# Performance work log

Hardware: AMD Instinct MI355X
Metric: run time of the kernel (lower is better)

## Reference

```python
import math
import jax, jax.numpy as jnp
import numpy as np

DIM = 1024
DIM_QK = 128
DIM_V = 1024
CHUNK = 512
NUM_BUCKETS = 32
MAX_DISTANCE = 128


def _rel_pos_bucket(n_q, n_k):
    # causal T5 bucketing on the chunk-local grid
    q_pos = jnp.arange(n_q, dtype=jnp.int32)
    k_pos = jnp.arange(n_k, dtype=jnp.int32)
    rel = k_pos[None, :] - q_pos[:, None]          # [i, j]
    n = jnp.maximum(-rel, 0)                        # distance into the past
    max_exact = NUM_BUCKETS // 2
    is_small = n < max_exact
    n_f = jnp.maximum(n, 1).astype(jnp.float32)     # safe log
    val_large = max_exact + jnp.log(n_f / max_exact) / math.log(MAX_DISTANCE / max_exact) * (NUM_BUCKETS - max_exact)
    val_large = jnp.minimum(val_large, NUM_BUCKETS - 1)
    bucket = jnp.where(is_small, n.astype(jnp.float32), val_large)
    return bucket.astype(jnp.int32)                 # [i, j]


def setup_inputs() -> dict:
    key = jax.random.key(0)
    ks = jax.random.split(key, 6)
    b, s = 8, 4096
    x = jax.random.normal(ks[0], (b, s, DIM), dtype=jnp.float32)
    # Dense(dim_qk) / Dense(dim_value) params (glorot-ish scale)
    Wqk = jax.random.normal(ks[1], (DIM, DIM_QK), dtype=jnp.float32) * (1.0 / math.sqrt(DIM))
    bqk = jnp.zeros((DIM_QK,), dtype=jnp.float32)
    Wv = jax.random.normal(ks[2], (DIM, DIM_V), dtype=jnp.float32) * (1.0 / math.sqrt(DIM))
    bv = jnp.zeros((DIM_V,), dtype=jnp.float32)
    # OffsetScale: gamma ~ N(0, 0.02), beta = 0, heads=2
    gamma = jax.random.normal(ks[3], (2, DIM_QK), dtype=jnp.float32) * 0.02
    beta = jnp.zeros((2, DIM_QK), dtype=jnp.float32)
    # T5 relative position bias embedding table [num_buckets, 1]
    rel_emb = jax.random.normal(ks[4], (NUM_BUCKETS, 1), dtype=jnp.float32) * 0.05
    return {"x": x, "Wqk": Wqk, "bqk": bqk, "Wv": Wv, "bv": bv,
            "gamma": gamma, "beta": beta, "rel_emb": rel_emb}


def reference(x, Wqk, bqk, Wv, bv, gamma, beta, rel_emb):
    b, s, dim = x.shape
    qk = jax.nn.swish(x @ Wqk + bqk)                # [b, s, dqk]
    v = jax.nn.swish(x @ Wv + bv)                   # [b, s, dv]
    # OffsetScale with 2 heads -> q, k
    os = qk[..., None, :] * gamma + beta            # [b, s, 2, dqk]
    q, k = os[..., 0, :], os[..., 1, :]
    # chunk: [b, nk, c, z] (block-diagonal attention within chunks)
    c = CHUNK
    nk = s // c
    q = q.reshape(b, nk, c, DIM_QK)
    k = k.reshape(b, nk, c, DIM_QK)
    vc = v.reshape(b, nk, c, DIM_V)
    scale = dim ** (-0.5)                           # NOTE: input dim, faithful to source
    sim = jnp.einsum('bkiz,bkjz->bkij', q, k) * scale
    # T5 rel-pos bias on the chunk-local (c, c) grid, scaled by dim_qk ** 0.5
    bucket = _rel_pos_bucket(c, c)
    bias = rel_emb[bucket, 0] * (DIM_QK ** 0.5)     # [c, c]
    sim = sim + bias
    # causal mask: strictly-upper (future) positions -> -inf
    future = jnp.triu(jnp.ones((c, c), dtype=bool), k=1)
    sim = jnp.where(future, -jnp.inf, sim)
    attn = jax.nn.softmax(sim, axis=-1)
    out = jnp.einsum('bkij,bkjz->bkiz', attn, vc)
    return out.reshape(b, s, DIM_V)
```

## Files before the change

kernel.cpp:

```cpp
#include <hip/hip_runtime.h>
#include <hip/hip_bf16.h>

using bf16x8 = __attribute__((ext_vector_type(8))) short;
using f32x4  = __attribute__((ext_vector_type(4))) float;
typedef unsigned short u16;

#define SEQ_TOT 32768
#define NCHUNK  64
#define SQRT128 11.313708498984761f

__device__ __forceinline__ u16 f2bf(float f) {
  unsigned u = __builtin_bit_cast(unsigned, f);
  u += 0x7fffu + ((u >> 16) & 1u);
  return (u16)(u >> 16);
}

__device__ __forceinline__ float swishf(float c) {
  return c / (1.0f + __expf(-c));
}

__global__ __launch_bounds__(256) void prep_wqkt(const float* __restrict__ Wqk,
                                                 u16* __restrict__ Wqkt) {
  int t = blockIdx.x * 256 + threadIdx.x;
  int n = t >> 10, k = t & 1023;
  Wqkt[t] = f2bf(Wqk[(size_t)k * 128 + n]);
}

__global__ __launch_bounds__(256) void prep_wvt(const float* __restrict__ Wv,
                                                u16* __restrict__ Wvt) {
  int t = blockIdx.x * 256 + threadIdx.x;
  int n = t >> 10, k = t & 1023;
  Wvt[t] = f2bf(Wv[(size_t)k * 1024 + n]);
}

__global__ __launch_bounds__(512) void prep_bias(const float* __restrict__ rel_emb,
                                                 float* __restrict__ bias_tab) {
  int d = threadIdx.x;
  int b;
  if (d < 16) {
    b = d;
  } else {
    float v = 16.0f + __logf((float)d * 0.0625f) * (16.0f / 2.0794415416798357f);
    b = (int)v;
    if (b > 31) b = 31;
  }
  bias_tab[d] = rel_emb[b] * SQRT128;
}

__global__ __launch_bounds__(256, 2) void proj_kernel(
    const float* __restrict__ x,
    const u16* __restrict__ Wqkt, const u16* __restrict__ Wvt,
    const float* __restrict__ bqk, const float* __restrict__ bv,
    const float* __restrict__ gamma, const float* __restrict__ beta,
    u16* __restrict__ qm, u16* __restrict__ km, u16* __restrict__ vt) {
  __shared__ u16 a_lds[128][40];
  __shared__ u16 b_lds[128][40];
  const int tid = threadIdx.x;
  const int lane = tid & 63;
  const int wid = tid >> 6;
  const int wm = wid >> 1, wn = wid & 1;
  const int m0 = blockIdx.x * 128;
  const int nb = blockIdx.y;
  const u16* Wt = (nb == 0) ? Wqkt : (Wvt + (size_t)(nb - 1) * 128 * 1024);

  f32x4 acc[4][4];
#pragma unroll
  for (int i = 0; i < 4; i++)
#pragma unroll
    for (int j = 0; j < 4; j++) acc[i][j] = f32x4{0.f, 0.f, 0.f, 0.f};

  const int srow = tid >> 1;
  const int shalf = (tid & 1) * 16;

  for (int kt = 0; kt < 32; ++kt) {
    const int k0 = kt * 32;
    __syncthreads();
    {
      const float* src = x + (size_t)(m0 + srow) * 1024 + k0 + shalf;
      float4 f0 = *(const float4*)(src);
      float4 f1 = *(const float4*)(src + 4);
      float4 f2 = *(const float4*)(src + 8);
      float4 f3 = *(const float4*)(src + 12);
      uint4 p0, p1;
      p0.x = f2bf(f0.x) | ((unsigned)f2bf(f0.y) << 16);
      p0.y = f2bf(f0.z) | ((unsigned)f2bf(f0.w) << 16);
      p0.z = f2bf(f1.x) | ((unsigned)f2bf(f1.y) << 16);
      p0.w = f2bf(f1.z) | ((unsigned)f2bf(f1.w) << 16);
      p1.x = f2bf(f2.x) | ((unsigned)f2bf(f2.y) << 16);
      p1.y = f2bf(f2.z) | ((unsigned)f2bf(f2.w) << 16);
      p1.z = f2bf(f3.x) | ((unsigned)f2bf(f3.y) << 16);
      p1.w = f2bf(f3.z) | ((unsigned)f2bf(f3.w) << 16);
      *(uint4*)&a_lds[srow][shalf] = p0;
      *(uint4*)&a_lds[srow][shalf + 8] = p1;
    }
    {
      const u16* src = Wt + (size_t)srow * 1024 + k0 + shalf;
      uint4 w0 = *(const uint4*)(src);
      uint4 w1 = *(const uint4*)(src + 8);
      *(uint4*)&b_lds[srow][shalf] = w0;
      *(uint4*)&b_lds[srow][shalf + 8] = w1;
    }
    __syncthreads();
    bf16x8 af[4], bfr[4];
#pragma unroll
    for (int mi = 0; mi < 4; mi++)
      af[mi] = *(const bf16x8*)&a_lds[wm * 64 + mi * 16 + (lane & 15)][8 * (lane >> 4)];
#pragma unroll
    for (int ni = 0; ni < 4; ni++)
      bfr[ni] = *(const bf16x8*)&b_lds[wn * 64 + ni * 16 + (lane & 15)][8 * (lane >> 4)];
#pragma unroll
    for (int mi = 0; mi < 4; mi++)
#pragma unroll
      for (int ni = 0; ni < 4; ni++)
        acc[mi][ni] = __builtin_amdgcn_mfma_f32_16x16x32_bf16(af[mi], bfr[ni], acc[mi][ni], 0, 0, 0);
  }

  if (nb == 0) {
#pragma unroll
    for (int ni = 0; ni < 4; ni++) {
      const int nn = wn * 64 + ni * 16 + (lane & 15);
      const float bb = bqk[nn];
      const float g0 = gamma[nn], g1 = gamma[128 + nn];
      const float be0 = beta[nn], be1 = beta[128 + nn];
#pragma unroll
      for (int mi = 0; mi < 4; mi++) {
#pragma unroll
        for (int r = 0; r < 4; r++) {
          const int m = m0 + wm * 64 + mi * 16 + (lane >> 4) * 4 + r;
          const float s = swishf(acc[mi][ni][r] + bb);
          qm[(size_t)m * 128 + nn] = f2bf(s * g0 + be0);
          km[(size_t)m * 128 + nn] = f2bf(s * g1 + be1);
        }
      }
    }
  } else {
#pragma unroll
    for (int ni = 0; ni < 4; ni++) {
      const int z = (nb - 1) * 128 + wn * 64 + ni * 16 + (lane & 15);
      const float bb = bv[z];
#pragma unroll
      for (int mi = 0; mi < 4; mi++) {
        const int m = m0 + wm * 64 + mi * 16 + (lane >> 4) * 4;
        const int chunkid = m >> 9;
        const int j = m & 511;
        ushort4 pk;
        pk.x = f2bf(swishf(acc[mi][ni][0] + bb));
        pk.y = f2bf(swishf(acc[mi][ni][1] + bb));
        pk.z = f2bf(swishf(acc[mi][ni][2] + bb));
        pk.w = f2bf(swishf(acc[mi][ni][3] + bb));
        *(ushort4*)&vt[((size_t)chunkid * 1024 + z) * 512 + j] = pk;
      }
    }
  }
}

__global__ __launch_bounds__(256, 2) void score_kernel(
    const u16* __restrict__ qm, const u16* __restrict__ km,
    const float* __restrict__ bias_tab, u16* __restrict__ P) {
  __shared__ u16 k_lds[64][136];
  const int tid = threadIdx.x;
  const int lane = tid & 63;
  const int wid = tid >> 6;
  const int qt = blockIdx.x;
  const int ch = blockIdx.y;

  bf16x8 qf[4];
  {
    const int r = ch * 512 + qt * 64 + wid * 16 + (lane & 15);
    const u16* qp = qm + (size_t)r * 128 + 8 * (lane >> 4);
#pragma unroll
    for (int kk = 0; kk < 4; kk++) qf[kk] = *(const bf16x8*)(qp + kk * 32);
  }

  f32x4 acc[32];
#pragma unroll
  for (int i = 0; i < 32; i++) acc[i] = f32x4{0.f, 0.f, 0.f, 0.f};

  const int srow = tid >> 2;
  const int soff = (tid & 3) * 32;

#pragma unroll
  for (int kt = 0; kt < 8; ++kt) {
    if (kt <= qt) {
      __syncthreads();
      {
        const u16* src = km + (size_t)(ch * 512 + kt * 64 + srow) * 128 + soff;
        uint4 w0 = *(const uint4*)(src);
        uint4 w1 = *(const uint4*)(src + 8);
        uint4 w2 = *(const uint4*)(src + 16);
        uint4 w3 = *(const uint4*)(src + 24);
        *(uint4*)&k_lds[srow][soff] = w0;
        *(uint4*)&k_lds[srow][soff + 8] = w1;
        *(uint4*)&k_lds[srow][soff + 16] = w2;
        *(uint4*)&k_lds[srow][soff + 24] = w3;
      }
      __syncthreads();
#pragma unroll
      for (int jt = 0; jt < 4; jt++) {
#pragma unroll
        for (int kk = 0; kk < 4; kk++) {
          bf16x8 bfr = *(const bf16x8*)&k_lds[jt * 16 + (lane & 15)][kk * 32 + 8 * (lane >> 4)];
          acc[kt * 4 + jt] =
              __builtin_amdgcn_mfma_f32_16x16x32_bf16(qf[kk], bfr, acc[kt * 4 + jt], 0, 0, 0);
        }
      }
    }
  }

  const float scale = 0.03125f;
  const int jbase = lane & 15;
  const int nct = (qt + 1) * 4;

#pragma unroll
  for (int r = 0; r < 4; r++) {
    const int i = qt * 64 + wid * 16 + (lane >> 4) * 4 + r;
    float mx = -INFINITY;
#pragma unroll
    for (int ct = 0; ct < 32; ++ct) {
      if (ct < nct) {
        const int j = ct * 16 + jbase;
        float val = (j <= i) ? (acc[ct][r] * scale + bias_tab[i - j]) : -INFINITY;
        acc[ct][r] = val;
        mx = fmaxf(mx, val);
      }
    }
#pragma unroll
    for (int d = 1; d < 16; d <<= 1) mx = fmaxf(mx, __shfl_xor(mx, d));
    float sum = 0.f;
#pragma unroll
    for (int ct = 0; ct < 32; ++ct) {
      if (ct < nct) {
        float e = __expf(acc[ct][r] - mx);
        acc[ct][r] = e;
        sum += e;
      }
    }
#pragma unroll
    for (int d = 1; d < 16; d <<= 1) sum += __shfl_xor(sum, d);
    const float inv = 1.0f / sum;
    const size_t base = ((size_t)ch * 512 + i) * 512;
#pragma unroll
    for (int ct = 0; ct < 32; ++ct) {
      u16 pv = (ct < nct) ? f2bf(acc[ct][r] * inv) : (u16)0;
      P[base + ct * 16 + jbase] = pv;
    }
  }
}

__global__ __launch_bounds__(256, 2) void out_kernel(
    const u16* __restrict__ P, const u16* __restrict__ vt,
    float* __restrict__ out) {
  __shared__ u16 a_lds[128][40];
  __shared__ u16 b_lds[128][40];
  const int tid = threadIdx.x;
  const int lane = tid & 63;
  const int wid = tid >> 6;
  const int wm = wid >> 1, wn = wid & 1;
  const int mb = blockIdx.x;
  const int nb = blockIdx.y;
  const int ch = blockIdx.z;
  const u16* Ab = P + (size_t)ch * 512 * 512 + (size_t)mb * 128 * 512;
  const u16* Bb = vt + (size_t)ch * 1024 * 512 + (size_t)nb * 128 * 512;

  f32x4 acc[4][4];
#pragma unroll
  for (int i = 0; i < 4; i++)
#pragma unroll
    for (int j = 0; j < 4; j++) acc[i][j] = f32x4{0.f, 0.f, 0.f, 0.f};

  const int srow = tid >> 1;
  const int shalf = (tid & 1) * 16;
  const int kend = (mb + 1) * 4;

  for (int kt = 0; kt < kend; ++kt) {
    const int k0 = kt * 32;
    __syncthreads();
    {
      const u16* s = Ab + (size_t)srow * 512 + k0 + shalf;
      uint4 w0 = *(const uint4*)(s);
      uint4 w1 = *(const uint4*)(s + 8);
      *(uint4*)&a_lds[srow][shalf] = w0;
      *(uint4*)&a_lds[srow][shalf + 8] = w1;
    }
    {
      const u16* s = Bb + (size_t)srow * 512 + k0 + shalf;
      uint4 w0 = *(const uint4*)(s);
      uint4 w1 = *(const uint4*)(s + 8);
      *(uint4*)&b_lds[srow][shalf] = w0;
      *(uint4*)&b_lds[srow][shalf + 8] = w1;
    }
    __syncthreads();
    bf16x8 af[4], bfr[4];
#pragma unroll
    for (int mi = 0; mi < 4; mi++)
      af[mi] = *(const bf16x8*)&a_lds[wm * 64 + mi * 16 + (lane & 15)][8 * (lane >> 4)];
#pragma unroll
    for (int ni = 0; ni < 4; ni++)
      bfr[ni] = *(const bf16x8*)&b_lds[wn * 64 + ni * 16 + (lane & 15)][8 * (lane >> 4)];
#pragma unroll
    for (int mi = 0; mi < 4; mi++)
#pragma unroll
      for (int ni = 0; ni < 4; ni++)
        acc[mi][ni] = __builtin_amdgcn_mfma_f32_16x16x32_bf16(af[mi], bfr[ni], acc[mi][ni], 0, 0, 0);
  }

#pragma unroll
  for (int ni = 0; ni < 4; ni++) {
    const int z = nb * 128 + wn * 64 + ni * 16 + (lane & 15);
#pragma unroll
    for (int mi = 0; mi < 4; mi++) {
#pragma unroll
      for (int r = 0; r < 4; r++) {
        const int i = mb * 128 + wm * 64 + mi * 16 + (lane >> 4) * 4 + r;
        out[((size_t)ch * 512 + i) * 1024 + z] = acc[mi][ni][r];
      }
    }
  }
}

extern "C" void kernel_launch(void* const* d_in, const int* in_sizes, int n_in,
                              void* d_out, int out_size, void* d_ws, size_t ws_size,
                              hipStream_t stream) {
  const float* x = (const float*)d_in[0];
  const float* Wqk = (const float*)d_in[1];
  const float* bqk = (const float*)d_in[2];
  const float* Wv = (const float*)d_in[3];
  const float* bv = (const float*)d_in[4];
  const float* gamma = (const float*)d_in[5];
  const float* beta = (const float*)d_in[6];
  const float* rel_emb = (const float*)d_in[7];

  char* ws = (char*)d_ws;
  u16* Wqkt = (u16*)(ws + 0);
  u16* Wvt = (u16*)(ws + 262144);
  float* bias_tab = (float*)(ws + 2359296);
  u16* qm = (u16*)(ws + 2361344);
  u16* km = (u16*)(ws + 10749952);
  u16* vt = (u16*)(ws + 19138560);
  u16* P = (u16*)(ws + 86247424);
  float* out = (float*)d_out;

  prep_wqkt<<<512, 256, 0, stream>>>(Wqk, Wqkt);
  prep_wvt<<<4096, 256, 0, stream>>>(Wv, Wvt);
  prep_bias<<<1, 512, 0, stream>>>(rel_emb, bias_tab);
  proj_kernel<<<dim3(256, 9), 256, 0, stream>>>(x, Wqkt, Wvt, bqk, bv, gamma, beta, qm, km, vt);
  score_kernel<<<dim3(8, 64), 256, 0, stream>>>(qm, km, bias_tab, P);
  out_kernel<<<dim3(4, 8, 64), 256, 0, stream>>>(P, vt, out);
}
```

Measured before the change: 486.1 us.

## Pre-convert x to bf16 and use direct global-to-LDS loads with swizzled tiles

Adds a prep kernel that converts x to bf16 once, into the output buffer used as scratch. Projection no longer re-reads fp32 x and re-converts it for each of the 9 column blocks, and its grid is transposed so blocks sharing an x row tile launch together. Both GEMM kernels now use global_load_lds with an XOR-swizzled 64-wide K tile instead of padded register-staged copies. The score kernel swaps MFMA operands so each lane owns a row, which cuts the shuffle reductions and lets P be written as 4-element vector stores. The cost is an extra full pass over x plus reliance on the output buffer as scratch before out_kernel overwrites it.

```diff
diff --git a/kernel.cpp b/kernel.cpp
--- a/kernel.cpp
+++ b/kernel.cpp
@@ -5,8 +5,6 @@
 using f32x4  = __attribute__((ext_vector_type(4))) float;
 typedef unsigned short u16;
 
-#define SEQ_TOT 32768
-#define NCHUNK  64
 #define SQRT128 11.313708498984761f
 
 __device__ __forceinline__ u16 f2bf(float f) {
@@ -17,6 +15,24 @@
 
 __device__ __forceinline__ float swishf(float c) {
   return c / (1.0f + __expf(-c));
+}
+
+__device__ __forceinline__ void gld16(const void* g, void* l) {
+  __builtin_amdgcn_global_load_lds((const __attribute__((address_space(1))) unsigned*)g,
+                                   (__attribute__((address_space(3))) unsigned*)l, 16, 0, 0);
+}
+
+__global__ __launch_bounds__(256) void prep_xb(const float* __restrict__ x,
+                                               u16* __restrict__ xb) {
+  size_t t = ((size_t)blockIdx.x * 256 + threadIdx.x) * 8;
+  float4 f0 = *(const float4*)(x + t);
+  float4 f1 = *(const float4*)(x + t + 4);
+  uint4 p;
+  p.x = f2bf(f0.x) | ((unsigned)f2bf(f0.y) << 16);
+  p.y = f2bf(f0.z) | ((unsigned)f2bf(f0.w) << 16);
+  p.z = f2bf(f1.x) | ((unsigned)f2bf(f1.y) << 16);
+  p.w = f2bf(f1.z) | ((unsigned)f2bf(f1.w) << 16);
+  *(uint4*)(xb + t) = p;
 }
 
 __global__ __launch_bounds__(256) void prep_wqkt(const float* __restrict__ Wqk,
@@ -48,19 +64,19 @@
 }
 
 __global__ __launch_bounds__(256, 2) void proj_kernel(
-    const float* __restrict__ x,
+    const u16* __restrict__ xb,
     const u16* __restrict__ Wqkt, const u16* __restrict__ Wvt,
     const float* __restrict__ bqk, const float* __restrict__ bv,
     const float* __restrict__ gamma, const float* __restrict__ beta,
     u16* __restrict__ qm, u16* __restrict__ km, u16* __restrict__ vt) {
-  __shared__ u16 a_lds[128][40];
-  __shared__ u16 b_lds[128][40];
+  __shared__ u16 a_lds[128 * 64];
+  __shared__ u16 b_lds[128 * 64];
   const int tid = threadIdx.x;
   const int lane = tid & 63;
-  const int wid = tid >> 6;
-  const int wm = wid >> 1, wn = wid & 1;
-  const int m0 = blockIdx.x * 128;
-  const int nb = blockIdx.y;
+  const int w = tid >> 6;
+  const int wm = w >> 1, wn = w & 1;
+  const int nb = blockIdx.x;
+  const int m0 = blockIdx.y * 128;
   const u16* Wt = (nb == 0) ? Wqkt : (Wvt + (size_t)(nb - 1) * 128 * 1024);
 
   f32x4 acc[4][4];
@@ -69,50 +85,41 @@
 #pragma unroll
     for (int j = 0; j < 4; j++) acc[i][j] = f32x4{0.f, 0.f, 0.f, 0.f};
 
-  const int srow = tid >> 1;
-  const int shalf = (tid & 1) * 16;
-
-  for (int kt = 0; kt < 32; ++kt) {
-    const int k0 = kt * 32;
+  const int srow_sub = w * 8 + (lane >> 3);
+  const int sbyte = (lane & 7) * 16;
+
+  for (int kt = 0; kt < 16; ++kt) {
+    const int k0 = kt * 64;
     __syncthreads();
-    {
-      const float* src = x + (size_t)(m0 + srow) * 1024 + k0 + shalf;
-      float4 f0 = *(const float4*)(src);
-      float4 f1 = *(const float4*)(src + 4);
-      float4 f2 = *(const float4*)(src + 8);
-      float4 f3 = *(const float4*)(src + 12);
-      uint4 p0, p1;
-      p0.x = f2bf(f0.x) | ((unsigned)f2bf(f0.y) << 16);
-      p0.y = f2bf(f0.z) | ((unsigned)f2bf(f0.w) << 16);
-      p0.z = f2bf(f1.x) | ((unsigned)f2bf(f1.y) << 16);
-      p0.w = f2bf(f1.z) | ((unsigned)f2bf(f1.w) << 16);
-      p1.x = f2bf(f2.x) | ((unsigned)f2bf(f2.y) << 16);
-      p1.y = f2bf(f2.z) | ((unsigned)f2bf(f2.w) << 16);
-      p1.z = f2bf(f3.x) | ((unsigned)f2bf(f3.y) << 16);
-      p1.w = f2bf(f3.z) | ((unsigned)f2bf(f3.w) << 16);
-      *(uint4*)&a_lds[srow][shalf] = p0;
-      *(uint4*)&a_lds[srow][shalf + 8] = p1;
-    }
-    {
-      const u16* src = Wt + (size_t)srow * 1024 + k0 + shalf;
-      uint4 w0 = *(const uint4*)(src);
-      uint4 w1 = *(const uint4*)(src + 8);
-      *(uint4*)&b_lds[srow][shalf] = w0;
-      *(uint4*)&b_lds[srow][shalf + 8] = w1;
+#pragma unroll
+    for (int i = 0; i < 4; ++i) {
+      const int row = i * 32 + srow_sub;
+      const int colb = sbyte ^ ((row & 7) << 4);
+      gld16(xb + (size_t)(m0 + row) * 1024 + k0 + (colb >> 1), &a_lds[(i * 4 + w) * 512]);
+      gld16(Wt + (size_t)row * 1024 + k0 + (colb >> 1), &b_lds[(i * 4 + w) * 512]);
     }
     __syncthreads();
-    bf16x8 af[4], bfr[4];
-#pragma unroll
-    for (int mi = 0; mi < 4; mi++)
-      af[mi] = *(const bf16x8*)&a_lds[wm * 64 + mi * 16 + (lane & 15)][8 * (lane >> 4)];
-#pragma unroll
-    for (int ni = 0; ni < 4; ni++)
-      bfr[ni] = *(const bf16x8*)&b_lds[wn * 64 + ni * 16 + (lane & 15)][8 * (lane >> 4)];
-#pragma unroll
-    for (int mi = 0; mi < 4; mi++)
-#pragma unroll
-      for (int ni = 0; ni < 4; ni++)
-        acc[mi][ni] = __builtin_amdgcn_mfma_f32_16x16x32_bf16(af[mi], bfr[ni], acc[mi][ni], 0, 0, 0);
+#pragma unroll
+    for (int kk = 0; kk < 2; ++kk) {
+      bf16x8 af[4], bfr[4];
+#pragma unroll
+      for (int mi = 0; mi < 4; mi++) {
+        const int row = wm * 64 + mi * 16 + (lane & 15);
+        const int byte_ = (kk * 64 + (lane >> 4) * 16) ^ ((row & 7) << 4);
+        af[mi] = *(const bf16x8*)((const char*)a_lds + row * 128 + byte_);
+      }
+#pragma unroll
+      for (int ni = 0; ni < 4; ni++) {
+        const int row = wn * 64 + ni * 16 + (lane & 15);
+        const int byte_ = (kk * 64 + (lane >> 4) * 16) ^ ((row & 7) << 4);
+        bfr[ni] = *(const bf16x8*)((const char*)b_lds + row * 128 + byte_);
+      }
+#pragma unroll
+      for (int mi = 0; mi < 4; mi++)
+#pragma unroll
+        for (int ni = 0; ni < 4; ni++)
+          acc[mi][ni] = __builtin_amdgcn_mfma_f32_16x16x32_bf16(af[mi], bfr[ni], acc[mi][ni], 0, 0, 0);
+    }
   }
 
   if (nb == 0) {
@@ -199,63 +206,74 @@
       for (int jt = 0; jt < 4; jt++) {
 #pragma unroll
         for (int kk = 0; kk < 4; kk++) {
-          bf16x8 bfr = *(const bf16x8*)&k_lds[jt * 16 + (lane & 15)][kk * 32 + 8 * (lane >> 4)];
+          bf16x8 kf = *(const bf16x8*)&k_lds[jt * 16 + (lane & 15)][kk * 32 + 8 * (lane >> 4)];
           acc[kt * 4 + jt] =
-              __builtin_amdgcn_mfma_f32_16x16x32_bf16(qf[kk], bfr, acc[kt * 4 + jt], 0, 0, 0);
+              __builtin_amdgcn_mfma_f32_16x16x32_bf16(kf, qf[kk], acc[kt * 4 + jt], 0, 0, 0);
         }
       }
     }
   }
 
   const float scale = 0.03125f;
-  const int jbase = lane & 15;
+  const int i = qt * 64 + wid * 16 + (lane & 15);
+  const int jb = (lane >> 4) * 4;
   const int nct = (qt + 1) * 4;
 
-#pragma unroll
-  for (int r = 0; r < 4; r++) {
-    const int i = qt * 64 + wid * 16 + (lane >> 4) * 4 + r;
-    float mx = -INFINITY;
-#pragma unroll
-    for (int ct = 0; ct < 32; ++ct) {
-      if (ct < nct) {
-        const int j = ct * 16 + jbase;
+  float mx = -INFINITY;
+#pragma unroll
+  for (int ct = 0; ct < 32; ++ct) {
+    if (ct < nct) {
+#pragma unroll
+      for (int r = 0; r < 4; r++) {
+        const int j = ct * 16 + jb + r;
         float val = (j <= i) ? (acc[ct][r] * scale + bias_tab[i - j]) : -INFINITY;
         acc[ct][r] = val;
         mx = fmaxf(mx, val);
       }
     }
-#pragma unroll
-    for (int d = 1; d < 16; d <<= 1) mx = fmaxf(mx, __shfl_xor(mx, d));
-    float sum = 0.f;
-#pragma unroll
-    for (int ct = 0; ct < 32; ++ct) {
-      if (ct < nct) {
+  }
+  mx = fmaxf(mx, __shfl_xor(mx, 16));
+  mx = fmaxf(mx, __shfl_xor(mx, 32));
+  float sum = 0.f;
+#pragma unroll
+  for (int ct = 0; ct < 32; ++ct) {
+    if (ct < nct) {
+#pragma unroll
+      for (int r = 0; r < 4; r++) {
         float e = __expf(acc[ct][r] - mx);
         acc[ct][r] = e;
         sum += e;
       }
     }
-#pragma unroll
-    for (int d = 1; d < 16; d <<= 1) sum += __shfl_xor(sum, d);
-    const float inv = 1.0f / sum;
-    const size_t base = ((size_t)ch * 512 + i) * 512;
-#pragma unroll
-    for (int ct = 0; ct < 32; ++ct) {
-      u16 pv = (ct < nct) ? f2bf(acc[ct][r] * inv) : (u16)0;
-      P[base + ct * 16 + jbase] = pv;
-    }
+  }
+  sum += __shfl_xor(sum, 16);
+  sum += __shfl_xor(sum, 32);
+  const float inv = 1.0f / sum;
+  const size_t base = ((size_t)ch * 512 + i) * 512 + jb;
+#pragma unroll
+  for (int ct = 0; ct < 32; ++ct) {
+    ushort4 pk;
+    if (ct < nct) {
+      pk.x = f2bf(acc[ct][0] * inv);
+      pk.y = f2bf(acc[ct][1] * inv);
+      pk.z = f2bf(acc[ct][2] * inv);
+      pk.w = f2bf(acc[ct][3] * inv);
+    } else {
+      pk.x = pk.y = pk.z = pk.w = 0;
+    }
+    *(ushort4*)&P[base + ct * 16] = pk;
   }
 }
 
 __global__ __launch_bounds__(256, 2) void out_kernel(
     const u16* __restrict__ P, const u16* __restrict__ vt,
     float* __restrict__ out) {
-  __shared__ u16 a_lds[128][40];
-  __shared__ u16 b_lds[128][40];
+  __shared__ u16 a_lds[128 * 64];
+  __shared__ u16 b_lds[128 * 64];
   const int tid = threadIdx.x;
   const int lane = tid & 63;
-  const int wid = tid >> 6;
-  const int wm = wid >> 1, wn = wid & 1;
+  const int w = tid >> 6;
+  const int wm = w >> 1, wn = w & 1;
   const int mb = blockIdx.x;
   const int nb = blockIdx.y;
   const int ch = blockIdx.z;
@@ -268,40 +286,42 @@
 #pragma unroll
     for (int j = 0; j < 4; j++) acc[i][j] = f32x4{0.f, 0.f, 0.f, 0.f};
 
-  const int srow = tid >> 1;
-  const int shalf = (tid & 1) * 16;
-  const int kend = (mb + 1) * 4;
+  const int srow_sub = w * 8 + (lane >> 3);
+  const int sbyte = (lane & 7) * 16;
+  const int kend = (mb + 1) * 2;
 
   for (int kt = 0; kt < kend; ++kt) {
-    const int k0 = kt * 32;
+    const int k0 = kt * 64;
     __syncthreads();
-    {
-      const u16* s = Ab + (size_t)srow * 512 + k0 + shalf;
-      uint4 w0 = *(const uint4*)(s);
-      uint4 w1 = *(const uint4*)(s + 8);
-      *(uint4*)&a_lds[srow][shalf] = w0;
-      *(uint4*)&a_lds[srow][shalf + 8] = w1;
-    }
-    {
-      const u16* s = Bb + (size_t)srow * 512 + k0 + shalf;
-      uint4 w0 = *(const uint4*)(s);
-      uint4 w1 = *(const uint4*)(s + 8);
-      *(uint4*)&b_lds[srow][shalf] = w0;
-      *(uint4*)&b_lds[srow][shalf + 8] = w1;
+#pragma unroll
+    for (int i = 0; i < 4; ++i) {
+      const int row = i * 32 + srow_sub;
+      const int colb = sbyte ^ ((row & 7) << 4);
+      gld16(Ab + (size_t)row * 512 + k0 + (colb >> 1), &a_lds[(i * 4 + w) * 512]);
+      gld16(Bb + (size_t)row * 512 + k0 + (colb >> 1), &b_lds[(i * 4 + w) * 512]);
     }
     __syncthreads();
-    bf16x8 af[4], bfr[4];
-#pragma unroll
-    for (int mi = 0; mi < 4; mi++)
-      af[mi] = *(const bf16x8*)&a_lds[wm * 64 + mi * 16 + (lane & 15)][8 * (lane >> 4)];
-#pragma unroll
-    for (int ni = 0; ni < 4; ni++)
-      bfr[ni] = *(const bf16x8*)&b_lds[wn * 64 + ni * 16 + (lane & 15)][8 * (lane >> 4)];
-#pragma unroll
-    for (int mi = 0; mi < 4; mi++)
-#pragma unroll
-      for (int ni = 0; ni < 4; ni++)
-        acc[mi][ni] = __builtin_amdgcn_mfma_f32_16x16x32_bf16(af[mi], bfr[ni], acc[mi][ni], 0, 0, 0);
+#pragma unroll
+    for (int kk = 0; kk < 2; ++kk) {
+      bf16x8 af[4], bfr[4];
+#pragma unroll
+      for (int mi = 0; mi < 4; mi++) {
+        const int row = wm * 64 + mi * 16 + (lane & 15);
+        const int byte_ = (kk * 64 + (lane >> 4) * 16) ^ ((row & 7) << 4);
+        af[mi] = *(const bf16x8*)((const char*)a_lds + row * 128 + byte_);
+      }
+#pragma unroll
+      for (int ni = 0; ni < 4; ni++) {
+        const int row = wn * 64 + ni * 16 + (lane & 15);
+        const int byte_ = (kk * 64 + (lane >> 4) * 16) ^ ((row & 7) << 4);
+        bfr[ni] = *(const bf16x8*)((const char*)b_lds + row * 128 + byte_);
+      }
+#pragma unroll
+      for (int mi = 0; mi < 4; mi++)
+#pragma unroll
+        for (int ni = 0; ni < 4; ni++)
+          acc[mi][ni] = __builtin_amdgcn_mfma_f32_16x16x32_bf16(af[mi], bfr[ni], acc[mi][ni], 0, 0, 0);
+    }
   }
 
 #pragma unroll
@@ -339,11 +359,13 @@
   u16* vt = (u16*)(ws + 19138560);
   u16* P = (u16*)(ws + 86247424);
   float* out = (float*)d_out;
-
+  u16* xb = (u16*)d_out;
+
+  prep_xb<<<16384, 256, 0, stream>>>(x, xb);
   prep_wqkt<<<512, 256, 0, stream>>>(Wqk, Wqkt);
   prep_wvt<<<4096, 256, 0, stream>>>(Wv, Wvt);
   prep_bias<<<1, 512, 0, stream>>>(rel_emb, bias_tab);
-  proj_kernel<<<dim3(256, 9), 256, 0, stream>>>(x, Wqkt, Wvt, bqk, bv, gamma, beta, qm, km, vt);
+  proj_kernel<<<dim3(9, 256), 256, 0, stream>>>(xb, Wqkt, Wvt, bqk, bv, gamma, beta, qm, km, vt);
   score_kernel<<<dim3(8, 64), 256, 0, stream>>>(qm, km, bias_tab, P);
   out_kernel<<<dim3(4, 8, 64), 256, 0, stream>>>(P, vt, out);
 }
```

Measured after the change: 466.6 us. 1.04x faster.
